# Kernel tuning notes

Hardware: AMD Instinct MI355X
Metric: run time of the kernel (lower is better)

The kernel has to match this reference:

```python
import jax, jax.numpy as jnp
import numpy as np

B, N, C, H = 4, 1024, 768, 12
HD = C // H
EPS = 1e-5


def setup_inputs() -> dict:
    key = jax.random.key(0)
    ks = jax.random.split(key, 6)
    before = jax.random.normal(ks[0], (B, N, C), dtype=jnp.float32)
    after = jax.random.normal(ks[1], (B, N, C), dtype=jnp.float32)
    W_qkv = jax.random.normal(ks[2], (3 * C, C), dtype=jnp.float32) * (1.0 / np.sqrt(C))
    ln_g = jnp.ones((HD,), dtype=jnp.float32)
    ln_b = jnp.zeros((HD,), dtype=jnp.float32)
    W_proj = jax.random.normal(ks[3], (C, C), dtype=jnp.float32) * (1.0 / np.sqrt(C))
    b_proj = jnp.zeros((C,), dtype=jnp.float32)
    return {"before": before, "after": after, "W_qkv": W_qkv, "ln_g": ln_g,
            "ln_b": ln_b, "W_proj": W_proj, "b_proj": b_proj}


def _qkv_norm(x, W_qkv, ln_g, ln_b):
    # x: [B,N,C] -> qkv: [3,B,H,N,hd] with LayerNorm over head_dim
    qkv = (x @ W_qkv.T).reshape(B, N, 3, H, HD).transpose(2, 0, 3, 1, 4)
    mu = jnp.mean(qkv, axis=-1, keepdims=True)
    var = jnp.var(qkv, axis=-1, keepdims=True)
    qkv = (qkv - mu) * jax.lax.rsqrt(var + EPS) * ln_g + ln_b
    return qkv[0], qkv[1], qkv[2]


def _cross_attn(q, k, v, scale, W_proj, b_proj):
    # q,k,v: [B,H,N,hd]
    attn = jax.nn.softmax(jnp.einsum('bhqd,bhkd->bhqk', q, k) * scale, axis=-1)
    ctx = jnp.einsum('bhqk,bhkd->bhqd', attn, v)  # [B,H,N,hd]
    ctx = ctx.transpose(0, 2, 1, 3).reshape(B, N, C)
    ctx = ctx @ W_proj.T + b_proj
    # NOTE: original adds q.reshape(B,N,C) WITHOUT transposing heads back; replicate faithfully.
    return ctx + q.reshape(B, N, C)


def reference(before, after, W_qkv, ln_g, ln_b, W_proj, b_proj):
    scale = HD ** (-0.5)
    q_b, k_b, v_b = _qkv_norm(before, W_qkv, ln_g, ln_b)
    q_a, k_a, v_a = _qkv_norm(after, W_qkv, ln_g, ln_b)
    context_a = _cross_attn(q_b, k_a, v_a, scale, W_proj, b_proj)
    context_b = _cross_attn(q_a, k_b, v_b, scale, W_proj, b_proj)
    return (context_b, context_a)
```

## Files before the change

### kernel.cpp

```cpp
#include <hip/hip_runtime.h>


typedef __bf16 bf16x8 __attribute__((ext_vector_type(8)));
typedef float  f32x4  __attribute__((ext_vector_type(4)));
typedef unsigned int u32x4 __attribute__((ext_vector_type(4)));
typedef unsigned short us;

#define MFMA16(a, b, c) __builtin_amdgcn_mfma_f32_16x16x32_bf16(a, b, c, 0, 0, 0)

__device__ __forceinline__ us f2bf(float f) {
  unsigned int u = __builtin_bit_cast(unsigned int, f);
  u += 0x7FFFu + ((u >> 16) & 1u);
  return (us)(u >> 16);
}
__device__ __forceinline__ float bf2f(us h) {
  unsigned int u = ((unsigned int)h) << 16;
  return __builtin_bit_cast(float, u);
}
__device__ __forceinline__ bf16x8 ld16(const us* p) {
  return __builtin_bit_cast(bf16x8, *(const u32x4*)p);
}

#define CH 136

__global__ __launch_bounds__(256) void k_convert(
    const float* __restrict__ before, const float* __restrict__ after,
    const float* __restrict__ wqkv, const float* __restrict__ wproj,
    us* __restrict__ ws) {
  int t = blockIdx.x * 256 + threadIdx.x;
  us* dst; int u;
  if (t < 786432)       { u = t;           dst = ws; }
  else if (t < 1007616) { u = t - 786432;  dst = ws + 6291456; }
  else                  { u = t - 1007616; dst = ws + 8060928; }
  int l15 = u & 15, c2 = u >> 4;
  int kc = c2 % 96, mt = c2 / 96;
  int row = mt * 16 + l15;
  const float* srow;
  if (t < 786432)       srow = row < 4096 ? before + (size_t)row * 768
                                          : after + (size_t)(row - 4096) * 768;
  else if (t < 1007616) srow = wqkv + (size_t)row * 768;
  else                  srow = wproj + (size_t)row * 768;
  const float4* s4 = (const float4*)(srow + kc * 8);
  float4 a = s4[0], b = s4[1];
  union { u32x4 v; us s[8]; } o;
  o.s[0] = f2bf(a.x); o.s[1] = f2bf(a.y); o.s[2] = f2bf(a.z); o.s[3] = f2bf(a.w);
  o.s[4] = f2bf(b.x); o.s[5] = f2bf(b.y); o.s[6] = f2bf(b.z); o.s[7] = f2bf(b.w);
  *(u32x4*)(dst + (size_t)c2 * 128 + l15 * 8) = o.v;
}

template <int MT, int MODE>
__global__ __launch_bounds__(256) void k_gemm(
    const us* __restrict__ A, const us* __restrict__ B, void* __restrict__ Cout,
    const us* __restrict__ qkvr, const float* __restrict__ bias,
    const float* __restrict__ g, const float* __restrict__ bb) {
  constexpr int MC = MT / 16;
  constexpr int AJ = MC / 2;
  constexpr int NITER = 12;
  __shared__ us As[MC * 8 * CH];
  __shared__ us Bs[64 * CH];
  const int tid = threadIdx.x, lane = tid & 63, w = tid >> 6;
  const int quad = lane >> 4, l15 = lane & 15;
  const int m0 = blockIdx.x * MT, n0 = blockIdx.y * 128;
  const int wm = (w >> 1) * (MT / 2), wn = (w & 1) * 64;
  f32x4 acc[AJ][4] = {};
  u32x4 ra[AJ], rb[4];

  auto load_regs = [&](int k0) {
#pragma unroll
    for (int j = 0; j < AJ; ++j) {
      int u = w * AJ + j;
      ra[j] = *(const u32x4*)(A + ((size_t)((m0 >> 4) + (u >> 1)) * 96
                                   + (k0 >> 3) + (u & 1) * 4) * 128 + lane * 8);
    }
#pragma unroll
    for (int j = 0; j < 4; ++j) {
      int u = w * 4 + j;
      rb[j] = *(const u32x4*)(B + ((size_t)((n0 >> 4) + (u >> 1)) * 96
                                   + (k0 >> 3) + (u & 1) * 4) * 128 + lane * 8);
    }
  };
  auto store_regs = [&]() {
#pragma unroll
    for (int j = 0; j < AJ; ++j) {
      int slot = (w * AJ + j) * 4 + (lane >> 4);
      *(u32x4*)(As + slot * CH + l15 * 8) = ra[j];
    }
#pragma unroll
    for (int j = 0; j < 4; ++j) {
      int slot = (w * 4 + j) * 4 + (lane >> 4);
      *(u32x4*)(Bs + slot * CH + l15 * 8) = rb[j];
    }
  };

  load_regs(0);
  store_regs();
  __syncthreads();

#pragma unroll
  for (int it = 0; it < NITER; ++it) {
    if (it + 1 < NITER) load_regs((it + 1) * 64);
#pragma unroll
    for (int ks = 0; ks < 2; ++ks) {
      bf16x8 af[AJ], bfr[4];
#pragma unroll
      for (int mf = 0; mf < AJ; ++mf)
        af[mf] = ld16(As + (((wm >> 4) + mf) * 8 + ks * 4 + quad) * CH + l15 * 8);
#pragma unroll
      for (int nf = 0; nf < 4; ++nf)
        bfr[nf] = ld16(Bs + (((wn >> 4) + nf) * 8 + ks * 4 + quad) * CH + l15 * 8);
#pragma unroll
      for (int mf = 0; mf < AJ; ++mf)
#pragma unroll
        for (int nf = 0; nf < 4; ++nf)
          acc[mf][nf] = MFMA16(af[mf], bfr[nf], acc[mf][nf]);
    }
    __syncthreads();
    if (it + 1 < NITER) {
      store_regs();
      __syncthreads();
    }
  }

  if (MODE == 0) {
    us* C = (us*)Cout;
    float gl[4], bl[4];
#pragma unroll
    for (int nf = 0; nf < 4; ++nf) { gl[nf] = g[nf * 16 + l15]; bl[nf] = bb[nf * 16 + l15]; }
#pragma unroll
    for (int mf = 0; mf < AJ; ++mf)
#pragma unroll
      for (int r = 0; r < 4; ++r) {
        float s1 = acc[mf][0][r] + acc[mf][1][r] + acc[mf][2][r] + acc[mf][3][r];
        float s2 = acc[mf][0][r] * acc[mf][0][r] + acc[mf][1][r] * acc[mf][1][r]
                 + acc[mf][2][r] * acc[mf][2][r] + acc[mf][3][r] * acc[mf][3][r];
#pragma unroll
        for (int o = 1; o < 16; o <<= 1) { s1 += __shfl_xor(s1, o); s2 += __shfl_xor(s2, o); }
        float mu = s1 * (1.0f / 64.0f);
        float var = s2 * (1.0f / 64.0f) - mu * mu;
        float sc = rsqrtf(var + 1e-5f);
        size_t cb = ((size_t)(((m0 + wm) >> 4) + mf) * 288 + ((n0 + wn) >> 3)
                     + (l15 >> 3)) * 128 + (quad * 4 + r) * 8 + (l15 & 7);
#pragma unroll
        for (int nf = 0; nf < 4; ++nf)
          C[cb + nf * 256] = f2bf((acc[mf][nf][r] - mu) * sc * gl[nf] + bl[nf]);
      }
  } else {
    float* C = (float*)Cout;
    const int cg = (n0 + wn) >> 6;
    float bl[4];
#pragma unroll
    for (int nf = 0; nf < 4; ++nf) bl[nf] = bias[n0 + wn + nf * 16 + l15];
#pragma unroll
    for (int mf = 0; mf < AJ; ++mf)
#pragma unroll
      for (int r = 0; r < 4; ++r) {
        int row = m0 + wm + mf * 16 + quad * 4 + r;
        int hf = row >> 12;
        int m4 = row & 4095;
        int b = m4 >> 10, i = m4 & 1023;
        int j = i * 12 + cg;
        int h = j >> 10, n = j & 1023;
        int qrow = ((hf ^ 1) << 12) + (b << 10) + n;
        size_t rb2 = ((size_t)(qrow >> 4) * 288 + h * 8 + (l15 >> 3)) * 128
                   + (qrow & 15) * 8 + (l15 & 7);
        size_t base = (size_t)row * 768 + n0 + wn + l15;
#pragma unroll
        for (int nf = 0; nf < 4; ++nf)
          C[base + nf * 16] = acc[mf][nf][r] + bl[nf] + bf2f(qkvr[rb2 + nf * 256]);
      }
  }
}

__global__ __launch_bounds__(256) void k_vt(const us* __restrict__ qkvr,
                                            us* __restrict__ vtg) {
  __shared__ us Ls[64 * 72];
  const int t = threadIdx.x;
  const int hi = blockIdx.x, kt = blockIdx.y;
  const int hf = hi / 48, bh = hi - hf * 48;
  const int b = bh / 12, h = bh - (bh / 12) * 12;
  const int qb16 = (hf * 4096 + b * 1024 + kt * 64) >> 4;
#pragma unroll
  for (int c0 = 0; c0 < 2; ++c0) {
    int slot = t + c0 * 256;
    int key = slot & 63, c = slot >> 6;
    size_t src = ((size_t)(qb16 + (key >> 4)) * 288 + 192 + h * 8 + c) * 128
               + (key & 15) * 8;
    *(u32x4*)(Ls + key * 72 + c * 8) = *(const u32x4*)(qkvr + src);
  }
  __syncthreads();
  us* vb = vtg + (size_t)hi * 65536;
#pragma unroll
  for (int c0 = 0; c0 < 2; ++c0) {
    int slot = t + c0 * 256;
    int d = (slot & 7) + ((slot >> 6) << 3);
    int kg = (slot >> 3) & 7;
    union { u32x4 v; us s[8]; } o;
#pragma unroll
    for (int j = 0; j < 8; ++j) o.s[j] = Ls[(kg * 8 + j) * 72 + d];
    *(u32x4*)(vb + ((size_t)(d >> 4) * 128 + kt * 8 + kg) * 128 + (d & 15) * 8) = o.v;
  }
}

__global__ __launch_bounds__(256) void k_attn(const us* __restrict__ qkvr,
                                              const us* __restrict__ vtg,
                                              us* __restrict__ ctx) {
  __shared__ us Ks[32 * CH];
  __shared__ us Vt[32 * CH];
  __shared__ us Ps[4][32 * 72];
  const int tid = threadIdx.x, lane = tid & 63, w = tid >> 6;
  const int quad = lane >> 4, l15 = lane & 15;
  const int hi = blockIdx.x, qt = blockIdx.y;
  const int hf = hi / 48, bh = hi - hf * 48;
  const int b = bh / 12, h = bh - (bh / 12) * 12;
  const int ihq = hf ^ 1, ihk = hf;
  const int r0 = qt * 128 + w * 32;
  const int qmt = (ihq * 4096 + b * 1024 + r0) >> 4;
  const int kb16 = (ihk * 4096 + b * 1024) >> 4;
  const us* vbase = vtg + (size_t)(ihk * 48 + b * 12 + h) * 65536;
  const float c1 = 0.125f * 1.44269504088896340736f;

  bf16x8 aq[2][2];
#pragma unroll
  for (int mf = 0; mf < 2; ++mf)
#pragma unroll
    for (int ks = 0; ks < 2; ++ks)
      aq[mf][ks] = ld16(qkvr + ((size_t)(qmt + mf) * 288 + h * 8 + ks * 4 + quad) * 128
                        + l15 * 8);

  u32x4 rk[2], rv[2];
  auto load_kv = [&](int kt) {
#pragma unroll
    for (int j = 0; j < 2; ++j) {
      int u = w * 2 + j;
      rk[j] = *(const u32x4*)(qkvr + ((size_t)(kb16 + kt * 4 + (u >> 1)) * 288
                                      + 96 + h * 8 + (u & 1) * 4) * 128 + lane * 8);
      rv[j] = *(const u32x4*)(vbase + ((size_t)(u >> 1) * 128 + kt * 8
                                       + (u & 1) * 4) * 128 + lane * 8);
    }
  };
  auto store_kv = [&]() {
#pragma unroll
    for (int j = 0; j < 2; ++j) {
      int slot = (w * 2 + j) * 4 + (lane >> 4);
      *(u32x4*)(Ks + slot * CH + l15 * 8) = rk[j];
      *(u32x4*)(Vt + slot * CH + l15 * 8) = rv[j];
    }
  };

  f32x4 O[2][4] = {};
  float lsum[2][4] = {};
  us* myP = Ps[w];

  load_kv(0);
  store_kv();
  __syncthreads();

  for (int kt = 0; kt < 16; ++kt) {
    if (kt + 1 < 16) load_kv(kt + 1);

    f32x4 s[2][4] = {};
#pragma unroll
    for (int ks = 0; ks < 2; ++ks)
#pragma unroll
      for (int nf = 0; nf < 4; ++nf) {
        bf16x8 bk = ld16(Ks + (nf * 8 + ks * 4 + quad) * CH + l15 * 8);
        s[0][nf] = MFMA16(aq[0][ks], bk, s[0][nf]);
        s[1][nf] = MFMA16(aq[1][ks], bk, s[1][nf]);
      }

#pragma unroll
    for (int mf = 0; mf < 2; ++mf)
#pragma unroll
      for (int r = 0; r < 4; ++r) {
        float p0 = __builtin_amdgcn_exp2f(s[mf][0][r] * c1);
        float p1 = __builtin_amdgcn_exp2f(s[mf][1][r] * c1);
        float p2 = __builtin_amdgcn_exp2f(s[mf][2][r] * c1);
        float p3 = __builtin_amdgcn_exp2f(s[mf][3][r] * c1);
        lsum[mf][r] += (p0 + p1) + (p2 + p3);
        int rowq = (mf * 16 + quad * 4 + r) * 72 + l15;
        myP[rowq]      = f2bf(p0);
        myP[rowq + 16] = f2bf(p1);
        myP[rowq + 32] = f2bf(p2);
        myP[rowq + 48] = f2bf(p3);
      }

#pragma unroll
    for (int k2 = 0; k2 < 2; ++k2) {
      bf16x8 pa0 = ld16(myP + l15 * 72 + k2 * 32 + quad * 8);
      bf16x8 pa1 = ld16(myP + (16 + l15) * 72 + k2 * 32 + quad * 8);
#pragma unroll
      for (int df = 0; df < 4; ++df) {
        bf16x8 bv = ld16(Vt + (df * 8 + k2 * 4 + quad) * CH + l15 * 8);
        O[0][df] = MFMA16(pa0, bv, O[0][df]);
        O[1][df] = MFMA16(pa1, bv, O[1][df]);
      }
    }

    __syncthreads();
    if (kt + 1 < 16) {
      store_kv();
      __syncthreads();
    }
  }

  const int omt = (hf * 4096 + b * 1024 + r0) >> 4;
#pragma unroll
  for (int mf = 0; mf < 2; ++mf)
#pragma unroll
    for (int r = 0; r < 4; ++r) {
      float l = lsum[mf][r];
#pragma unroll
      for (int o = 1; o < 16; o <<= 1) l += __shfl_xor(l, o);
      float inv = 1.0f / l;
      size_t cb = ((size_t)(omt + mf) * 96 + h * 8 + (l15 >> 3)) * 128
                + (quad * 4 + r) * 8 + (l15 & 7);
#pragma unroll
      for (int df = 0; df < 4; ++df)
        ctx[cb + df * 256] = f2bf(O[mf][df][r] * inv);
    }
}

extern "C" void kernel_launch(void* const* d_in, const int* in_sizes, int n_in,
                              void* d_out, int out_size, void* d_ws, size_t ws_size,
                              hipStream_t stream) {
  (void)in_sizes; (void)n_in; (void)out_size; (void)ws_size;
  const float* before = (const float*)d_in[0];
  const float* after  = (const float*)d_in[1];
  const float* wqkv   = (const float*)d_in[2];
  const float* lng    = (const float*)d_in[3];
  const float* lnb    = (const float*)d_in[4];
  const float* wproj  = (const float*)d_in[5];
  const float* bproj  = (const float*)d_in[6];
  float* out = (float*)d_out;
  us* ws  = (us*)d_ws;
  us* xbt = ws;
  us* vtg = ws;
  us* wqt = ws + 6291456;
  us* wpt = ws + 8060928;
  us* qkvr = ws + 8650752;
  us* ctx  = ws + 27525120;

  k_convert<<<4224, 256, 0, stream>>>(before, after, wqkv, wproj, ws);
  k_gemm<128, 0><<<dim3(64, 18), 256, 0, stream>>>(
      xbt, wqt, (void*)qkvr, nullptr, nullptr, lng, lnb);
  k_vt<<<dim3(96, 16), 256, 0, stream>>>(qkvr, vtg);
  k_attn<<<dim3(96, 8), 256, 0, stream>>>(qkvr, vtg, ctx);
  k_gemm<64, 1><<<dim3(128, 6), 256, 0, stream>>>(
      ctx, wpt, (void*)out, qkvr, bproj, nullptr, nullptr);
}
```

Measured before the change: 212.4 us.

## Fuse V transpose into QKV GEMM epilogue and use lightweight LDS barriers

The QKV GEMM epilogue now writes the V columns straight into the transposed per-head layout that attention consumes, which removes the separate k_vt kernel launch and its extra read and write of V. Q and K are stored in a narrower 192-column-block buffer, and the attention and projection kernels have their indexing updated to match. __syncthreads is replaced with an inline-asm s_waitcnt lgkmcnt(0) plus s_barrier, which drops the wait on outstanding global loads at each barrier. The trade-off is V stores of 8 bytes that are less coalesced, and a barrier that depends on the compiler not needing a vmcnt wait at those points.

```diff
diff --git a/kernel.cpp b/kernel.cpp
--- a/kernel.cpp
+++ b/kernel.cpp
@@ -19,6 +19,9 @@
 }
 __device__ __forceinline__ bf16x8 ld16(const us* p) {
   return __builtin_bit_cast(bf16x8, *(const u32x4*)p);
+}
+__device__ __forceinline__ void barrier_lds() {
+  asm volatile("s_waitcnt lgkmcnt(0)\n\ts_barrier" ::: "memory");
 }
 
 #define CH 136
@@ -48,21 +51,15 @@
   *(u32x4*)(dst + (size_t)c2 * 128 + l15 * 8) = o.v;
 }
 
-template <int MT, int MODE>
-__global__ __launch_bounds__(256) void k_gemm(
-    const us* __restrict__ A, const us* __restrict__ B, void* __restrict__ Cout,
-    const us* __restrict__ qkvr, const float* __restrict__ bias,
-    const float* __restrict__ g, const float* __restrict__ bb) {
-  constexpr int MC = MT / 16;
-  constexpr int AJ = MC / 2;
+template <int MT>
+__device__ __forceinline__ void gemm_mainloop(
+    const us* __restrict__ A, const us* __restrict__ B,
+    int m0, int n0, us* As, us* Bs, f32x4 (&acc)[MT / 32][4]) {
+  constexpr int AJ = MT / 32;
   constexpr int NITER = 12;
-  __shared__ us As[MC * 8 * CH];
-  __shared__ us Bs[64 * CH];
   const int tid = threadIdx.x, lane = tid & 63, w = tid >> 6;
   const int quad = lane >> 4, l15 = lane & 15;
-  const int m0 = blockIdx.x * MT, n0 = blockIdx.y * 128;
   const int wm = (w >> 1) * (MT / 2), wn = (w & 1) * 64;
-  f32x4 acc[AJ][4] = {};
   u32x4 ra[AJ], rb[4];
 
   auto load_regs = [&](int k0) {
@@ -82,19 +79,19 @@
   auto store_regs = [&]() {
 #pragma unroll
     for (int j = 0; j < AJ; ++j) {
-      int slot = (w * AJ + j) * 4 + (lane >> 4);
+      int slot = (w * AJ + j) * 4 + quad;
       *(u32x4*)(As + slot * CH + l15 * 8) = ra[j];
     }
 #pragma unroll
     for (int j = 0; j < 4; ++j) {
-      int slot = (w * 4 + j) * 4 + (lane >> 4);
+      int slot = (w * 4 + j) * 4 + quad;
       *(u32x4*)(Bs + slot * CH + l15 * 8) = rb[j];
     }
   };
 
   load_regs(0);
   store_regs();
-  __syncthreads();
+  barrier_lds();
 
 #pragma unroll
   for (int it = 0; it < NITER; ++it) {
@@ -114,20 +111,33 @@
         for (int nf = 0; nf < 4; ++nf)
           acc[mf][nf] = MFMA16(af[mf], bfr[nf], acc[mf][nf]);
     }
-    __syncthreads();
+    barrier_lds();
     if (it + 1 < NITER) {
       store_regs();
-      __syncthreads();
+      barrier_lds();
     }
   }
-
-  if (MODE == 0) {
-    us* C = (us*)Cout;
-    float gl[4], bl[4];
-#pragma unroll
-    for (int nf = 0; nf < 4; ++nf) { gl[nf] = g[nf * 16 + l15]; bl[nf] = bb[nf * 16 + l15]; }
-#pragma unroll
-    for (int mf = 0; mf < AJ; ++mf)
+}
+
+__global__ __launch_bounds__(256) void k_gemm_qkv(
+    const us* __restrict__ A, const us* __restrict__ B, us* __restrict__ Cqk,
+    us* __restrict__ Vg, const float* __restrict__ g, const float* __restrict__ bb) {
+  __shared__ us As[64 * CH];
+  __shared__ us Bs[64 * CH];
+  const int lane = threadIdx.x & 63, w = threadIdx.x >> 6;
+  const int quad = lane >> 4, l15 = lane & 15;
+  const int m0 = blockIdx.x * 128, n0 = blockIdx.y * 128;
+  const int wm = (w >> 1) * 64, wn = (w & 1) * 64;
+  f32x4 acc[4][4] = {};
+  gemm_mainloop<128>(A, B, m0, n0, As, Bs, acc);
+
+  float gl[4], bl[4];
+#pragma unroll
+  for (int nf = 0; nf < 4; ++nf) { gl[nf] = g[nf * 16 + l15]; bl[nf] = bb[nf * 16 + l15]; }
+
+  if ((n0 + wn) < 1536) {
+#pragma unroll
+    for (int mf = 0; mf < 4; ++mf)
 #pragma unroll
       for (int r = 0; r < 4; ++r) {
         float s1 = acc[mf][0][r] + acc[mf][1][r] + acc[mf][2][r] + acc[mf][3][r];
@@ -138,67 +148,81 @@
         float mu = s1 * (1.0f / 64.0f);
         float var = s2 * (1.0f / 64.0f) - mu * mu;
         float sc = rsqrtf(var + 1e-5f);
-        size_t cb = ((size_t)(((m0 + wm) >> 4) + mf) * 288 + ((n0 + wn) >> 3)
+        size_t cb = ((size_t)(((m0 + wm) >> 4) + mf) * 192 + ((n0 + wn) >> 3)
                      + (l15 >> 3)) * 128 + (quad * 4 + r) * 8 + (l15 & 7);
 #pragma unroll
         for (int nf = 0; nf < 4; ++nf)
-          C[cb + nf * 256] = f2bf((acc[mf][nf][r] - mu) * sc * gl[nf] + bl[nf]);
+          Cqk[cb + nf * 256] = f2bf((acc[mf][nf][r] - mu) * sc * gl[nf] + bl[nf]);
       }
   } else {
-    float* C = (float*)Cout;
-    const int cg = (n0 + wn) >> 6;
-    float bl[4];
-#pragma unroll
-    for (int nf = 0; nf < 4; ++nf) bl[nf] = bias[n0 + wn + nf * 16 + l15];
-#pragma unroll
-    for (int mf = 0; mf < AJ; ++mf)
+    const int h = ((n0 + wn) - 1536) >> 6;
+#pragma unroll
+    for (int mf = 0; mf < 4; ++mf) {
+      int mrow = m0 + wm + mf * 16;
+      int s = mrow >> 12, b2 = (mrow >> 10) & 3;
+      int K0 = mrow & 1023;
+      us* vb = Vg + (size_t)(s * 48 + b2 * 12 + h) * 65536;
+      float vv[4][4];
 #pragma unroll
       for (int r = 0; r < 4; ++r) {
-        int row = m0 + wm + mf * 16 + quad * 4 + r;
-        int hf = row >> 12;
-        int m4 = row & 4095;
-        int b = m4 >> 10, i = m4 & 1023;
-        int j = i * 12 + cg;
-        int h = j >> 10, n = j & 1023;
-        int qrow = ((hf ^ 1) << 12) + (b << 10) + n;
-        size_t rb2 = ((size_t)(qrow >> 4) * 288 + h * 8 + (l15 >> 3)) * 128
-                   + (qrow & 15) * 8 + (l15 & 7);
-        size_t base = (size_t)row * 768 + n0 + wn + l15;
+        float s1 = acc[mf][0][r] + acc[mf][1][r] + acc[mf][2][r] + acc[mf][3][r];
+        float s2 = acc[mf][0][r] * acc[mf][0][r] + acc[mf][1][r] * acc[mf][1][r]
+                 + acc[mf][2][r] * acc[mf][2][r] + acc[mf][3][r] * acc[mf][3][r];
+#pragma unroll
+        for (int o = 1; o < 16; o <<= 1) { s1 += __shfl_xor(s1, o); s2 += __shfl_xor(s2, o); }
+        float mu = s1 * (1.0f / 64.0f);
+        float var = s2 * (1.0f / 64.0f) - mu * mu;
+        float sc = rsqrtf(var + 1e-5f);
 #pragma unroll
         for (int nf = 0; nf < 4; ++nf)
-          C[base + nf * 16] = acc[mf][nf][r] + bl[nf] + bf2f(qkvr[rb2 + nf * 256]);
-      }
+          vv[nf][r] = (acc[mf][nf][r] - mu) * sc * gl[nf] + bl[nf];
+      }
+#pragma unroll
+      for (int nf = 0; nf < 4; ++nf) {
+        ushort4 o4;
+        o4.x = f2bf(vv[nf][0]); o4.y = f2bf(vv[nf][1]);
+        o4.z = f2bf(vv[nf][2]); o4.w = f2bf(vv[nf][3]);
+        *(ushort4*)(vb + ((size_t)nf * 128 + (K0 >> 3) + (quad >> 1)) * 128
+                    + l15 * 8 + (quad & 1) * 4) = o4;
+      }
+    }
   }
 }
 
-__global__ __launch_bounds__(256) void k_vt(const us* __restrict__ qkvr,
-                                            us* __restrict__ vtg) {
-  __shared__ us Ls[64 * 72];
-  const int t = threadIdx.x;
-  const int hi = blockIdx.x, kt = blockIdx.y;
-  const int hf = hi / 48, bh = hi - hf * 48;
-  const int b = bh / 12, h = bh - (bh / 12) * 12;
-  const int qb16 = (hf * 4096 + b * 1024 + kt * 64) >> 4;
-#pragma unroll
-  for (int c0 = 0; c0 < 2; ++c0) {
-    int slot = t + c0 * 256;
-    int key = slot & 63, c = slot >> 6;
-    size_t src = ((size_t)(qb16 + (key >> 4)) * 288 + 192 + h * 8 + c) * 128
-               + (key & 15) * 8;
-    *(u32x4*)(Ls + key * 72 + c * 8) = *(const u32x4*)(qkvr + src);
-  }
-  __syncthreads();
-  us* vb = vtg + (size_t)hi * 65536;
-#pragma unroll
-  for (int c0 = 0; c0 < 2; ++c0) {
-    int slot = t + c0 * 256;
-    int d = (slot & 7) + ((slot >> 6) << 3);
-    int kg = (slot >> 3) & 7;
-    union { u32x4 v; us s[8]; } o;
-#pragma unroll
-    for (int j = 0; j < 8; ++j) o.s[j] = Ls[(kg * 8 + j) * 72 + d];
-    *(u32x4*)(vb + ((size_t)(d >> 4) * 128 + kt * 8 + kg) * 128 + (d & 15) * 8) = o.v;
-  }
+__global__ __launch_bounds__(256) void k_gemm_proj(
+    const us* __restrict__ A, const us* __restrict__ B, float* __restrict__ C,
+    const us* __restrict__ qkvr, const float* __restrict__ bias) {
+  __shared__ us As[32 * CH];
+  __shared__ us Bs[64 * CH];
+  const int lane = threadIdx.x & 63, w = threadIdx.x >> 6;
+  const int quad = lane >> 4, l15 = lane & 15;
+  const int m0 = blockIdx.x * 64, n0 = blockIdx.y * 128;
+  const int wm = (w >> 1) * 32, wn = (w & 1) * 64;
+  f32x4 acc[2][4] = {};
+  gemm_mainloop<64>(A, B, m0, n0, As, Bs, acc);
+
+  const int cg = (n0 + wn) >> 6;
+  float bl[4];
+#pragma unroll
+  for (int nf = 0; nf < 4; ++nf) bl[nf] = bias[n0 + wn + nf * 16 + l15];
+#pragma unroll
+  for (int mf = 0; mf < 2; ++mf)
+#pragma unroll
+    for (int r = 0; r < 4; ++r) {
+      int row = m0 + wm + mf * 16 + quad * 4 + r;
+      int hf = row >> 12;
+      int m4 = row & 4095;
+      int b = m4 >> 10, i = m4 & 1023;
+      int j = i * 12 + cg;
+      int h = j >> 10, n = j & 1023;
+      int qrow = ((hf ^ 1) << 12) + (b << 10) + n;
+      size_t rb2 = ((size_t)(qrow >> 4) * 192 + h * 8 + (l15 >> 3)) * 128
+                 + (qrow & 15) * 8 + (l15 & 7);
+      size_t base = (size_t)row * 768 + n0 + wn + l15;
+#pragma unroll
+      for (int nf = 0; nf < 4; ++nf)
+        C[base + nf * 16] = acc[mf][nf][r] + bl[nf] + bf2f(qkvr[rb2 + nf * 256]);
+    }
 }
 
 __global__ __launch_bounds__(256) void k_attn(const us* __restrict__ qkvr,
@@ -224,7 +248,7 @@
   for (int mf = 0; mf < 2; ++mf)
 #pragma unroll
     for (int ks = 0; ks < 2; ++ks)
-      aq[mf][ks] = ld16(qkvr + ((size_t)(qmt + mf) * 288 + h * 8 + ks * 4 + quad) * 128
+      aq[mf][ks] = ld16(qkvr + ((size_t)(qmt + mf) * 192 + h * 8 + ks * 4 + quad) * 128
                         + l15 * 8);
 
   u32x4 rk[2], rv[2];
@@ -232,7 +256,7 @@
 #pragma unroll
     for (int j = 0; j < 2; ++j) {
       int u = w * 2 + j;
-      rk[j] = *(const u32x4*)(qkvr + ((size_t)(kb16 + kt * 4 + (u >> 1)) * 288
+      rk[j] = *(const u32x4*)(qkvr + ((size_t)(kb16 + kt * 4 + (u >> 1)) * 192
                                       + 96 + h * 8 + (u & 1) * 4) * 128 + lane * 8);
       rv[j] = *(const u32x4*)(vbase + ((size_t)(u >> 1) * 128 + kt * 8
                                        + (u & 1) * 4) * 128 + lane * 8);
@@ -241,7 +265,7 @@
   auto store_kv = [&]() {
 #pragma unroll
     for (int j = 0; j < 2; ++j) {
-      int slot = (w * 2 + j) * 4 + (lane >> 4);
+      int slot = (w * 2 + j) * 4 + quad;
       *(u32x4*)(Ks + slot * CH + l15 * 8) = rk[j];
       *(u32x4*)(Vt + slot * CH + l15 * 8) = rv[j];
     }
@@ -253,7 +277,7 @@
 
   load_kv(0);
   store_kv();
-  __syncthreads();
+  barrier_lds();
 
   for (int kt = 0; kt < 16; ++kt) {
     if (kt + 1 < 16) load_kv(kt + 1);
@@ -296,10 +320,10 @@
       }
     }
 
-    __syncthreads();
+    barrier_lds();
     if (kt + 1 < 16) {
       store_kv();
-      __syncthreads();
+      barrier_lds();
     }
   }
 
@@ -333,18 +357,15 @@
   const float* bproj  = (const float*)d_in[6];
   float* out = (float*)d_out;
   us* ws  = (us*)d_ws;
-  us* xbt = ws;
-  us* vtg = ws;
-  us* wqt = ws + 6291456;
-  us* wpt = ws + 8060928;
+  us* xbt  = ws;
+  us* wqt  = ws + 6291456;
+  us* wpt  = ws + 8060928;
   us* qkvr = ws + 8650752;
+  us* vtg  = ws + 21233664;
   us* ctx  = ws + 27525120;
 
   k_convert<<<4224, 256, 0, stream>>>(before, after, wqkv, wproj, ws);
-  k_gemm<128, 0><<<dim3(64, 18), 256, 0, stream>>>(
-      xbt, wqt, (void*)qkvr, nullptr, nullptr, lng, lnb);
-  k_vt<<<dim3(96, 16), 256, 0, stream>>>(qkvr, vtg);
+  k_gemm_qkv<<<dim3(64, 18), 256, 0, stream>>>(xbt, wqt, qkvr, vtg, lng, lnb);
   k_attn<<<dim3(96, 8), 256, 0, stream>>>(qkvr, vtg, ctx);
-  k_gemm<64, 1><<<dim3(128, 6), 256, 0, stream>>>(
-      ctx, wpt, (void*)out, qkvr, bproj, nullptr, nullptr);
-}
+  k_gemm_proj<<<dim3(128, 6), 256, 0, stream>>>(ctx, wpt, out, qkvr, bproj);
+}
```

Result: faster. 194.3 us (-8.5%).
